# Kernel tuning notes

Measured on AMD Instinct MI355X. Metric: run time of the kernel, lower is better.

## Reference

```python
import jax, jax.numpy as jnp
import numpy as np

B, S, E, H = 16, 512, 768, 12
D = E // H
SCALING = 1.0 / np.sqrt(D * 1.0)  # scaling_factor = 1


def setup_inputs() -> dict:
    key = jax.random.key(0)
    ks = jax.random.split(key, 8)
    query = jax.random.normal(ks[0], (B, S, E), dtype=jnp.float32)
    key_in = jax.random.normal(ks[1], (B, S, E), dtype=jnp.float32)
    value = jax.random.normal(ks[2], (B, S, E), dtype=jnp.float32)
    key_padding_mask = jax.random.randint(ks[3], (B, S), 0, 2).astype(jnp.bool_)
    attn_bias = jax.random.normal(ks[4], (B, H, S, S), dtype=jnp.float32)
    # Learned params. NOTE: original code applies wq to q, k AND v (wk/wv unused).
    Wq = jax.random.normal(ks[5], (E, E), dtype=jnp.float32) * (1.0 / np.sqrt(E))
    bq = jnp.zeros((E,), dtype=jnp.float32)
    Wo = jax.random.normal(ks[6], (E, E), dtype=jnp.float32) * (1.0 / np.sqrt(E))
    bo = jnp.zeros((E,), dtype=jnp.float32)
    return {"query": query, "key": key_in, "value": value,
            "key_padding_mask": key_padding_mask, "attn_bias": attn_bias,
            "Wq": Wq, "bq": bq, "Wo": Wo, "bo": bo}


def _split_heads(x):
    # [B,S,E] -> [B,H,S,D]
    return x.reshape(B, S, H, D).transpose(0, 2, 1, 3)


def reference(query, key, value, key_padding_mask, attn_bias, Wq, bq, Wo, bo):
    q = (query @ Wq + bq) * jnp.asarray(SCALING, query.dtype)
    k = key @ Wq + bq      # faithful: wq used for k and v in the source
    v = value @ Wq + bq
    q, k, v = _split_heads(q), _split_heads(k), _split_heads(v)  # [B,H,S,D]
    w = jnp.einsum('bhtd,bhsd->bhts', q, k)                      # [B,H,T,S]
    w = jnp.where(key_padding_mask[:, None, None, :], -jnp.inf, w)
    w = w + attn_bias
    attn = jax.nn.softmax(w, axis=-1)  # dropout is no-op (training=False)
    o = jnp.einsum('bhts,bhsd->bhtd', attn, v)
    o = o.transpose(0, 2, 1, 3).reshape(B, S, E)
    o = o @ Wo + bo
    attn_weights = w.reshape(B * H, S, S)
    return (o, attn_weights, attn.reshape(B * H, S, S))
```

## Files before the change

### kernel.cpp

```cpp
#include <hip/hip_runtime.h>
#include <cmath>

#define BB 16
#define SS 512
#define EE 768
#define HH 12
#define DD 64
#define NBH (BB*HH)

#define MASK_NEG (-1.0e30f)

__device__ __forceinline__ unsigned short bf16_rn(float x) {
    unsigned u = __float_as_uint(x);
    u += 0x7FFFu + ((u >> 16) & 1u);
    return (unsigned short)(u >> 16);
}
__device__ __forceinline__ float bf16_tof(unsigned short h) {
    return __uint_as_float(((unsigned)h) << 16);
}

typedef __attribute__((ext_vector_type(8))) short bf16x8;
typedef __attribute__((ext_vector_type(4))) float f32x4;
typedef __attribute__((ext_vector_type(4))) unsigned short u16x4;

__global__ __launch_bounds__(256) void conv_w_kernel(
    const float* __restrict__ Wq, const float* __restrict__ Wo,
    unsigned short* __restrict__ wtq, unsigned short* __restrict__ wto)
{
    const float* __restrict__ W = blockIdx.z ? Wo : Wq;
    unsigned short* __restrict__ wt = blockIdx.z ? wto : wtq;
    const int k = blockIdx.x * 256 + threadIdx.x;
    const int n = blockIdx.y;
    const float x = W[(size_t)k * EE + n];
    const unsigned short h = bf16_rn(x);
    const float r = x - bf16_tof(h);
    const unsigned short m = bf16_rn(r);
    const float l2 = r - bf16_tof(m);
    const unsigned short l = bf16_rn(l2);
    const size_t PL = (size_t)EE * EE;
    wt[0 * PL + (size_t)n * EE + k] = h;
    wt[1 * PL + (size_t)n * EE + k] = m;
    wt[2 * PL + (size_t)n * EE + k] = l;
}

__global__ __launch_bounds__(256) void split_gemm_qkv_kernel(
    const float* __restrict__ Xq, const float* __restrict__ Xk,
    const float* __restrict__ Xv, const unsigned short* __restrict__ wt,
    const float* __restrict__ bvec,
    unsigned short* __restrict__ qp, unsigned short* __restrict__ kp,
    unsigned short* __restrict__ vtp)
{
    const int z = blockIdx.z;
    const float* __restrict__ X = (z == 1) ? Xk : (z == 2) ? Xv : Xq;
    const float scale = (z == 0) ? 0.125f : 1.0f;

    const int m0 = blockIdx.x * 128;
    const int n0 = blockIdx.y * 128;

    __shared__ __align__(16) unsigned short lds[4 * 4096];
    const int AH = 0, AL = 4096, BH = 8192, BL = 12288;

    const int tid = threadIdx.x;
    const int srow = tid >> 2;
    const int sg   = tid & 3;
    const int wv = tid >> 6;
    const int wr = wv >> 1, wc = wv & 1;
    const int lane = tid & 63;
    const int l15 = lane & 15, lg = lane >> 4;

    const size_t PL = (size_t)EE * EE;
    const size_t PS = (size_t)NBH * SS * DD;

    f32x4 acc[4][4];
#pragma unroll
    for (int i = 0; i < 4; ++i)
#pragma unroll
        for (int j = 0; j < 4; ++j) acc[i][j] = (f32x4){0.f, 0.f, 0.f, 0.f};

    float4 xf[2][2];
    bf16x8 wh[2], wl[2];

#define QKV_LOAD(K0)                                                          \
    {                                                                         \
        _Pragma("unroll")                                                     \
        for (int half = 0; half < 2; ++half) {                                \
            const int row = srow + 64 * half;                                 \
            const float* xp = &X[(size_t)(m0 + row) * EE + (K0) + sg * 8];    \
            xf[half][0] = *reinterpret_cast<const float4*>(xp);               \
            xf[half][1] = *reinterpret_cast<const float4*>(xp + 4);           \
            const size_t bo = (size_t)(n0 + row) * EE + (K0) + sg * 8;        \
            wh[half] = *reinterpret_cast<const bf16x8*>(&wt[0 * PL + bo]);    \
            wl[half] = *reinterpret_cast<const bf16x8*>(&wt[1 * PL + bo]);    \
        }                                                                     \
    }

    QKV_LOAD(0);

#pragma unroll 1
    for (int k0 = 0; k0 < EE; k0 += 32) {
        __syncthreads();
#pragma unroll
        for (int half = 0; half < 2; ++half) {
            const int row = srow + 64 * half;
            const float xs[8] = {xf[half][0].x, xf[half][0].y, xf[half][0].z, xf[half][0].w,
                                 xf[half][1].x, xf[half][1].y, xf[half][1].z, xf[half][1].w};
            bf16x8 hv, mv;
#pragma unroll
            for (int e = 0; e < 8; ++e) {
                const float x = xs[e];
                const unsigned short h = bf16_rn(x);
                const unsigned short m = bf16_rn(x - bf16_tof(h));
                hv[e] = (short)h;
                mv[e] = (short)m;
            }
            const int o = row * 32 + sg * 8;
            *reinterpret_cast<bf16x8*>(&lds[AH + o]) = hv;
            *reinterpret_cast<bf16x8*>(&lds[AL + o]) = mv;
            *reinterpret_cast<bf16x8*>(&lds[BH + o]) = wh[half];
            *reinterpret_cast<bf16x8*>(&lds[BL + o]) = wl[half];
        }
        __syncthreads();

        if (k0 + 32 < EE) QKV_LOAD(k0 + 32);

        bf16x8 ah[4], al[4];
#pragma unroll
        for (int i = 0; i < 4; ++i) {
            const int o = (wr * 64 + i * 16 + l15) * 32 + lg * 8;
            ah[i] = *reinterpret_cast<const bf16x8*>(&lds[AH + o]);
            al[i] = *reinterpret_cast<const bf16x8*>(&lds[AL + o]);
        }
#pragma unroll
        for (int j = 0; j < 4; ++j) {
            const int o = (wc * 64 + j * 16 + l15) * 32 + lg * 8;
            const bf16x8 bh = *reinterpret_cast<const bf16x8*>(&lds[BH + o]);
            const bf16x8 bl = *reinterpret_cast<const bf16x8*>(&lds[BL + o]);
#pragma unroll
            for (int i = 0; i < 4; ++i) {
                acc[i][j] = __builtin_amdgcn_mfma_f32_16x16x32_bf16(ah[i], bh, acc[i][j], 0, 0, 0);
                acc[i][j] = __builtin_amdgcn_mfma_f32_16x16x32_bf16(ah[i], bl, acc[i][j], 0, 0, 0);
                acc[i][j] = __builtin_amdgcn_mfma_f32_16x16x32_bf16(al[i], bh, acc[i][j], 0, 0, 0);
                acc[i][j] = __builtin_amdgcn_mfma_f32_16x16x32_bf16(al[i], bl, acc[i][j], 0, 0, 0);
            }
        }
    }
#undef QKV_LOAD

    unsigned short* __restrict__ dstp = (z == 0) ? qp : kp;
#pragma unroll
    for (int j = 0; j < 4; ++j) {
        const int n = n0 + wc * 64 + j * 16 + l15;
        const float bvn = bvec[n];
        const int h = n >> 6, d = n & 63;
#pragma unroll
        for (int i = 0; i < 4; ++i) {
            const int mb = m0 + wr * 64 + i * 16 + lg * 4;
#pragma unroll
            for (int r = 0; r < 4; ++r) {
                const int m = mb + r;
                const int bh_ = (m >> 9) * HH + h;
                const int srow_ = m & 511;
                const float val = (acc[i][j][r] + bvn) * scale;
                const unsigned short hi = bf16_rn(val);
                const unsigned short lo = bf16_rn(val - bf16_tof(hi));
                if (z == 2) {
                    const size_t o = ((size_t)bh_ * DD + d) * SS + srow_;
                    vtp[o] = hi;
                    vtp[o + PS] = lo;
                } else {
                    const size_t o = ((size_t)bh_ * SS + srow_) * DD + d;
                    dstp[o] = hi;
                    dstp[o + PS] = lo;
                }
            }
        }
    }
}

__global__ __launch_bounds__(256) void flash_attn_kernel(
    const unsigned short* __restrict__ qp, const unsigned short* __restrict__ kp,
    const unsigned short* __restrict__ vt, const unsigned char* __restrict__ mask,
    const float* __restrict__ bias, float* __restrict__ wout,
    float* __restrict__ ohb, float* __restrict__ stat_m,
    float* __restrict__ stat_inv)
{
    const int bh = blockIdx.y;
    const int b = bh / HH, h = bh % HH;
    const int t0 = blockIdx.x * 64;
    const int tid = threadIdx.x;
    const int wv = tid >> 6;
    const int lane = tid & 63, l15 = lane & 15, lg = lane >> 4;
    const size_t PS = (size_t)NBH * SS * DD;

    __shared__ __align__(16) unsigned short kbuf[2 * 64 * 68];
    __shared__ __align__(16) unsigned short vbuf[2 * 64 * 68];
    __shared__ __align__(16) unsigned short pbuf[4 * 2 * 16 * 68];

    bf16x8 bqh[2], bql[2];
    {
        const unsigned short* qbase = &qp[((size_t)bh * SS + t0 + wv * 16) * DD];
#pragma unroll
        for (int kc = 0; kc < 2; ++kc) {
            const size_t o = (size_t)l15 * DD + kc * 32 + lg * 8;
            bqh[kc] = *reinterpret_cast<const bf16x8*>(&qbase[o]);
            bql[kc] = *reinterpret_cast<const bf16x8*>(&qbase[o + PS]);
        }
    }

    float rm = -3.0e38f, rs = 0.0f;

    f32x4 oac[4];
#pragma unroll
    for (int j = 0; j < 4; ++j) oac[j] = (f32x4){0.f, 0.f, 0.f, 0.f};

    const int t = t0 + wv * 16 + l15;

    const unsigned short* __restrict__ kb0 = &kp[(size_t)bh * SS * DD];
    const unsigned short* __restrict__ vb0 = &vt[(size_t)bh * DD * SS];
    const int srow2 = tid >> 3, sg2 = (tid & 7) * 8;

    bf16x8 krh[2], krl[2], vrh[2], vrl[2];

#define FA_LOADKV(SC)                                                         \
    {                                                                         \
        _Pragma("unroll")                                                     \
        for (int rep = 0; rep < 2; ++rep) {                                   \
            const int row = srow2 + rep * 32;                                 \
            krh[rep] = *reinterpret_cast<const bf16x8*>(                      \
                &kb0[(size_t)((SC) + row) * DD + sg2]);                       \
            krl[rep] = *reinterpret_cast<const bf16x8*>(                      \
                &kb0[(size_t)((SC) + row) * DD + sg2 + PS]);                  \
            vrh[rep] = *reinterpret_cast<const bf16x8*>(                      \
                &vb0[(size_t)row * SS + (SC) + sg2]);                         \
            vrl[rep] = *reinterpret_cast<const bf16x8*>(                      \
                &vb0[(size_t)row * SS + (SC) + sg2 + PS]);                    \
        }                                                                     \
    }

    FA_LOADKV(0);

#pragma unroll 1
    for (int c = 0; c < 8; ++c) {
        const int sc = c * 64;
        __syncthreads();

#pragma unroll
        for (int rep = 0; rep < 2; ++rep) {
            const int row = srow2 + rep * 32;
            *reinterpret_cast<bf16x8*>(&kbuf[row * 68 + sg2]) = krh[rep];
            *reinterpret_cast<bf16x8*>(&kbuf[64 * 68 + row * 68 + sg2]) = krl[rep];
            *reinterpret_cast<bf16x8*>(&vbuf[row * 68 + sg2]) = vrh[rep];
            *reinterpret_cast<bf16x8*>(&vbuf[64 * 68 + row * 68 + sg2]) = vrl[rep];
        }
        __syncthreads();

        if (c < 7) FA_LOADKV(sc + 64);

        float4 bvr[4];
        uchar4 mkr[4];
#pragma unroll
        for (int i = 0; i < 4; ++i) {
            const int s = sc + i * 16 + lg * 4;
            bvr[i] = *reinterpret_cast<const float4*>(&bias[((size_t)bh * SS + t) * SS + s]);
            mkr[i] = *reinterpret_cast<const uchar4*>(&mask[b * SS + s]);
        }

        f32x4 ws[4];
#pragma unroll
        for (int i = 0; i < 4; ++i) ws[i] = (f32x4){0.f, 0.f, 0.f, 0.f};
#pragma unroll
        for (int kc = 0; kc < 2; ++kc) {
#pragma unroll
            for (int i = 0; i < 4; ++i) {
                const int o = (i * 16 + l15) * 68 + kc * 32 + lg * 8;
                const bf16x8 ah = *reinterpret_cast<const bf16x8*>(&kbuf[o]);
                const bf16x8 al = *reinterpret_cast<const bf16x8*>(&kbuf[64 * 68 + o]);
                ws[i] = __builtin_amdgcn_mfma_f32_16x16x32_bf16(ah, bqh[kc], ws[i], 0, 0, 0);
                ws[i] = __builtin_amdgcn_mfma_f32_16x16x32_bf16(ah, bql[kc], ws[i], 0, 0, 0);
                ws[i] = __builtin_amdgcn_mfma_f32_16x16x32_bf16(al, bqh[kc], ws[i], 0, 0, 0);
                ws[i] = __builtin_amdgcn_mfma_f32_16x16x32_bf16(al, bql[kc], ws[i], 0, 0, 0);
            }
        }

        float mx = -3.0e38f;
#pragma unroll
        for (int i = 0; i < 4; ++i) {
            const int s = sc + i * 16 + lg * 4;
            const size_t go = ((size_t)bh * SS + t) * SS + s;
            float4 w4;
            w4.x = mkr[i].x ? MASK_NEG : ws[i][0] + bvr[i].x;
            w4.y = mkr[i].y ? MASK_NEG : ws[i][1] + bvr[i].y;
            w4.z = mkr[i].z ? MASK_NEG : ws[i][2] + bvr[i].z;
            w4.w = mkr[i].w ? MASK_NEG : ws[i][3] + bvr[i].w;
            *reinterpret_cast<float4*>(&wout[go]) = w4;
            ws[i][0] = w4.x; ws[i][1] = w4.y; ws[i][2] = w4.z; ws[i][3] = w4.w;
            mx = fmaxf(mx, fmaxf(fmaxf(w4.x, w4.y), fmaxf(w4.z, w4.w)));
        }
        mx = fmaxf(mx, __shfl_xor(mx, 16));
        mx = fmaxf(mx, __shfl_xor(mx, 32));

        const float m_new = fmaxf(rm, mx);
        float sm = 0.0f;
#pragma unroll
        for (int i = 0; i < 4; ++i)
#pragma unroll
            for (int r = 0; r < 4; ++r) sm += __expf(ws[i][r] - m_new);
        sm += __shfl_xor(sm, 16);
        sm += __shfl_xor(sm, 32);
        const float scl = __expf(rm - m_new);
        rs = rs * scl + sm;
        rm = m_new;

        unsigned short* pw = &pbuf[(wv * 2) * 16 * 68];
#pragma unroll
        for (int i = 0; i < 4; ++i) {
            float4 p4;
            p4.x = __expf(ws[i][0] - m_new);
            p4.y = __expf(ws[i][1] - m_new);
            p4.z = __expf(ws[i][2] - m_new);
            p4.w = __expf(ws[i][3] - m_new);
            u16x4 hv, lv;
            hv.x = bf16_rn(p4.x); lv.x = bf16_rn(p4.x - bf16_tof(hv.x));
            hv.y = bf16_rn(p4.y); lv.y = bf16_rn(p4.y - bf16_tof(hv.y));
            hv.z = bf16_rn(p4.z); lv.z = bf16_rn(p4.z - bf16_tof(hv.z));
            hv.w = bf16_rn(p4.w); lv.w = bf16_rn(p4.w - bf16_tof(hv.w));
            const int po = l15 * 68 + i * 16 + lg * 4;
            *reinterpret_cast<u16x4*>(&pw[po]) = hv;
            *reinterpret_cast<u16x4*>(&pw[16 * 68 + po]) = lv;
        }

        float sclr[4];
#pragma unroll
        for (int r = 0; r < 4; ++r) sclr[r] = __shfl(scl, lg * 4 + r);
#pragma unroll
        for (int j = 0; j < 4; ++j)
#pragma unroll
            for (int r = 0; r < 4; ++r) oac[j][r] *= sclr[r];

#pragma unroll
        for (int kc = 0; kc < 2; ++kc) {
            const int ko = kc * 32 + lg * 8;
            const bf16x8 pah = *reinterpret_cast<const bf16x8*>(&pw[l15 * 68 + ko]);
            const bf16x8 pal = *reinterpret_cast<const bf16x8*>(&pw[16 * 68 + l15 * 68 + ko]);
#pragma unroll
            for (int j = 0; j < 4; ++j) {
                const int o = (j * 16 + l15) * 68 + ko;
                const bf16x8 vh = *reinterpret_cast<const bf16x8*>(&vbuf[o]);
                const bf16x8 vl = *reinterpret_cast<const bf16x8*>(&vbuf[64 * 68 + o]);
                oac[j] = __builtin_amdgcn_mfma_f32_16x16x32_bf16(pah, vh, oac[j], 0, 0, 0);
                oac[j] = __builtin_amdgcn_mfma_f32_16x16x32_bf16(pah, vl, oac[j], 0, 0, 0);
                oac[j] = __builtin_amdgcn_mfma_f32_16x16x32_bf16(pal, vh, oac[j], 0, 0, 0);
                oac[j] = __builtin_amdgcn_mfma_f32_16x16x32_bf16(pal, vl, oac[j], 0, 0, 0);
            }
        }
    }
#undef FA_LOADKV

    const float inv = 1.0f / rs;
    if (lg == 0) {
        stat_m[(size_t)bh * SS + t] = rm;
        stat_inv[(size_t)bh * SS + t] = inv;
    }
    float invr[4];
#pragma unroll
    for (int r = 0; r < 4; ++r) invr[r] = __shfl(inv, lg * 4 + r);
#pragma unroll
    for (int j = 0; j < 4; ++j)
#pragma unroll
        for (int r = 0; r < 4; ++r) {
            const int tr = t0 + wv * 16 + lg * 4 + r;
            ohb[((size_t)b * SS + tr) * EE + h * DD + j * 16 + l15] = oac[j][r] * invr[r];
        }
}

__global__ __launch_bounds__(256) void finish_kernel(
    const float* __restrict__ X, const unsigned short* __restrict__ wt,
    const float* __restrict__ bvec, float* __restrict__ dflat,
    const float* __restrict__ win, const float* __restrict__ stat_m,
    const float* __restrict__ stat_inv, float* __restrict__ attn)
{
    __shared__ __align__(16) unsigned short lds[6 * 4096];

    if (blockIdx.x >= 384) {
        const int nb = gridDim.x - 384;
        const size_t total = (size_t)NBH * SS * (SS / 4);
        for (size_t g = (size_t)(blockIdx.x - 384) * 256 + threadIdx.x; g < total;
             g += (size_t)nb * 256) {
            const size_t row = g >> 7;
            const float m_ = stat_m[row];
            const float iv = stat_inv[row];
            const float4 w4 = reinterpret_cast<const float4*>(win)[g];
            float4 p4;
            p4.x = __expf(w4.x - m_) * iv;
            p4.y = __expf(w4.y - m_) * iv;
            p4.z = __expf(w4.z - m_) * iv;
            p4.w = __expf(w4.w - m_) * iv;
            reinterpret_cast<float4*>(attn)[g] = p4;
        }
        return;
    }

    const int m0 = (blockIdx.x & 63) * 128;
    const int n0 = (blockIdx.x >> 6) * 128;

    const int AH = 0, AM = 4096, AL = 8192, BH = 12288, BM = 16384, BL = 20480;

    const int tid = threadIdx.x;
    const int srow = tid >> 2;
    const int sg   = tid & 3;
    const int wv = tid >> 6;
    const int wr = wv >> 1, wc = wv & 1;
    const int lane = tid & 63;
    const int l15 = lane & 15, lg = lane >> 4;
    const size_t PL = (size_t)EE * EE;

    f32x4 acc[4][4];
#pragma unroll
    for (int i = 0; i < 4; ++i)
#pragma unroll
        for (int j = 0; j < 4; ++j) acc[i][j] = (f32x4){0.f, 0.f, 0.f, 0.f};

#pragma unroll 1
    for (int k0 = 0; k0 < EE; k0 += 32) {
#pragma unroll
        for (int half = 0; half < 2; ++half) {
            const int row = srow + 64 * half;
            const float* xp = &X[(size_t)(m0 + row) * EE + k0 + sg * 8];
            const float4 f0 = *reinterpret_cast<const float4*>(xp);
            const float4 f1 = *reinterpret_cast<const float4*>(xp + 4);
            const float xs[8] = {f0.x, f0.y, f0.z, f0.w, f1.x, f1.y, f1.z, f1.w};
            bf16x8 hv, mv, lv;
#pragma unroll
            for (int e = 0; e < 8; ++e) {
                const float x = xs[e];
                const unsigned short h = bf16_rn(x);
                const float r = x - bf16_tof(h);
                const unsigned short m = bf16_rn(r);
                const float l2 = r - bf16_tof(m);
                hv[e] = (short)h;
                mv[e] = (short)m;
                lv[e] = (short)bf16_rn(l2);
            }
            const int o = row * 32 + sg * 8;
            *reinterpret_cast<bf16x8*>(&lds[AH + o]) = hv;
            *reinterpret_cast<bf16x8*>(&lds[AM + o]) = mv;
            *reinterpret_cast<bf16x8*>(&lds[AL + o]) = lv;

            const size_t bo = (size_t)(n0 + row) * EE + k0 + sg * 8;
            *reinterpret_cast<bf16x8*>(&lds[BH + o]) =
                *reinterpret_cast<const bf16x8*>(&wt[0 * PL + bo]);
            *reinterpret_cast<bf16x8*>(&lds[BM + o]) =
                *reinterpret_cast<const bf16x8*>(&wt[1 * PL + bo]);
            *reinterpret_cast<bf16x8*>(&lds[BL + o]) =
                *reinterpret_cast<const bf16x8*>(&wt[2 * PL + bo]);
        }
        __syncthreads();

        bf16x8 ah[4], am[4], al[4];
#pragma unroll
        for (int i = 0; i < 4; ++i) {
            const int o = (wr * 64 + i * 16 + l15) * 32 + lg * 8;
            ah[i] = *reinterpret_cast<const bf16x8*>(&lds[AH + o]);
            am[i] = *reinterpret_cast<const bf16x8*>(&lds[AM + o]);
            al[i] = *reinterpret_cast<const bf16x8*>(&lds[AL + o]);
        }
#pragma unroll
        for (int j = 0; j < 4; ++j) {
            const int o = (wc * 64 + j * 16 + l15) * 32 + lg * 8;
            const bf16x8 bh = *reinterpret_cast<const bf16x8*>(&lds[BH + o]);
            const bf16x8 bm = *reinterpret_cast<const bf16x8*>(&lds[BM + o]);
            const bf16x8 bl = *reinterpret_cast<const bf16x8*>(&lds[BL + o]);
#pragma unroll
            for (int i = 0; i < 4; ++i) {
                acc[i][j] = __builtin_amdgcn_mfma_f32_16x16x32_bf16(ah[i], bh, acc[i][j], 0, 0, 0);
                acc[i][j] = __builtin_amdgcn_mfma_f32_16x16x32_bf16(ah[i], bm, acc[i][j], 0, 0, 0);
                acc[i][j] = __builtin_amdgcn_mfma_f32_16x16x32_bf16(am[i], bh, acc[i][j], 0, 0, 0);
                acc[i][j] = __builtin_amdgcn_mfma_f32_16x16x32_bf16(ah[i], bl, acc[i][j], 0, 0, 0);
                acc[i][j] = __builtin_amdgcn_mfma_f32_16x16x32_bf16(al[i], bh, acc[i][j], 0, 0, 0);
                acc[i][j] = __builtin_amdgcn_mfma_f32_16x16x32_bf16(am[i], bm, acc[i][j], 0, 0, 0);
            }
        }
        __syncthreads();
    }

#pragma unroll
    for (int j = 0; j < 4; ++j) {
        const int n = n0 + wc * 64 + j * 16 + l15;
        const float bvn = bvec[n];
#pragma unroll
        for (int i = 0; i < 4; ++i) {
            const int mb = m0 + wr * 64 + i * 16 + lg * 4;
#pragma unroll
            for (int r = 0; r < 4; ++r)
                dflat[(size_t)(mb + r) * EE + n] = acc[i][j][r] + bvn;
        }
    }
}

__global__ __launch_bounds__(256) void proj_kernel(
    const float* __restrict__ Xq, const float* __restrict__ Xk,
    const float* __restrict__ Xv, const float* __restrict__ W,
    const float* __restrict__ bvec, float* __restrict__ qb,
    float* __restrict__ kb, float* __restrict__ vb)
{
    const int z = blockIdx.z;
    const float* __restrict__ X = (z == 0) ? Xq : (z == 1) ? Xk : Xv;
    float* __restrict__ Dst = (z == 0) ? qb : (z == 1) ? kb : vb;
    const float scale = (z == 0) ? 0.125f : 1.0f;

    const int m0 = blockIdx.x * 128;
    const int n0 = blockIdx.y * 128;

    __shared__ float As[16][128];
    __shared__ float Bs[16][128];

    const int tid = threadIdx.x;
    const int ty = tid >> 4, tx = tid & 15;

    float acc[8][8];
#pragma unroll
    for (int i = 0; i < 8; ++i)
#pragma unroll
        for (int j = 0; j < 8; ++j) acc[i][j] = 0.0f;

    const int arow = tid >> 1;
    const int ak   = (tid & 1) * 8;
    const int brow = tid >> 4;
    const int bn   = (tid & 15) * 8;

    for (int k0 = 0; k0 < EE; k0 += 16) {
        const float4* ap = reinterpret_cast<const float4*>(&X[(size_t)(m0 + arow) * EE + k0 + ak]);
        float4 a0 = ap[0], a1 = ap[1];
        As[ak + 0][arow] = a0.x; As[ak + 1][arow] = a0.y;
        As[ak + 2][arow] = a0.z; As[ak + 3][arow] = a0.w;
        As[ak + 4][arow] = a1.x; As[ak + 5][arow] = a1.y;
        As[ak + 6][arow] = a1.z; As[ak + 7][arow] = a1.w;

        const float4* bp = reinterpret_cast<const float4*>(&W[(size_t)(k0 + brow) * EE + n0 + bn]);
        float4 b0 = bp[0], b1 = bp[1];
        *reinterpret_cast<float4*>(&Bs[brow][bn])     = b0;
        *reinterpret_cast<float4*>(&Bs[brow][bn + 4]) = b1;
        __syncthreads();

#pragma unroll
        for (int kk = 0; kk < 16; ++kk) {
            float4 aA = *reinterpret_cast<const float4*>(&As[kk][ty * 8]);
            float4 aB = *reinterpret_cast<const float4*>(&As[kk][ty * 8 + 4]);
            float4 bA = *reinterpret_cast<const float4*>(&Bs[kk][tx * 8]);
            float4 bB = *reinterpret_cast<const float4*>(&Bs[kk][tx * 8 + 4]);
            float av[8] = {aA.x, aA.y, aA.z, aA.w, aB.x, aB.y, aB.z, aB.w};
            float bv[8] = {bA.x, bA.y, bA.z, bA.w, bB.x, bB.y, bB.z, bB.w};
#pragma unroll
            for (int i = 0; i < 8; ++i)
#pragma unroll
                for (int j = 0; j < 8; ++j)
                    acc[i][j] = fmaf(av[i], bv[j], acc[i][j]);
        }
        __syncthreads();
    }

    const int nbase = n0 + tx * 8;
    float bq8[8];
    {
        float4 c0 = *reinterpret_cast<const float4*>(&bvec[nbase]);
        float4 c1 = *reinterpret_cast<const float4*>(&bvec[nbase + 4]);
        bq8[0]=c0.x; bq8[1]=c0.y; bq8[2]=c0.z; bq8[3]=c0.w;
        bq8[4]=c1.x; bq8[5]=c1.y; bq8[6]=c1.z; bq8[7]=c1.w;
    }
    const int hh = nbase >> 6;
    const int dd = nbase & 63;
#pragma unroll
    for (int i = 0; i < 8; ++i) {
        const int m = m0 + ty * 8 + i;
        const int bidx = m >> 9;
        const int srow = m & 511;
        float* dst = &Dst[(((size_t)bidx * HH + hh) * SS + srow) * DD + dd];
        float4 v0, v1;
        v0.x = (acc[i][0] + bq8[0]) * scale;
        v0.y = (acc[i][1] + bq8[1]) * scale;
        v0.z = (acc[i][2] + bq8[2]) * scale;
        v0.w = (acc[i][3] + bq8[3]) * scale;
        v1.x = (acc[i][4] + bq8[4]) * scale;
        v1.y = (acc[i][5] + bq8[5]) * scale;
        v1.z = (acc[i][6] + bq8[6]) * scale;
        v1.w = (acc[i][7] + bq8[7]) * scale;
        *reinterpret_cast<float4*>(dst)     = v0;
        *reinterpret_cast<float4*>(dst + 4) = v1;
    }
}

__global__ __launch_bounds__(256) void scores_kernel(
    const float* __restrict__ qb, const float* __restrict__ kb,
    const unsigned char* __restrict__ mask,
    const float* __restrict__ bias, float* __restrict__ wout)
{
    const int bh = blockIdx.z;
    const int b  = bh / HH;
    const int t0 = blockIdx.y * 128;
    const int s0 = blockIdx.x * 128;

    __shared__ float As[16][128];
    __shared__ float Bs[16][128];

    const int tid = threadIdx.x;
    const int ty = tid >> 4, tx = tid & 15;

    float acc[8][8];
#pragma unroll
    for (int i = 0; i < 8; ++i)
#pragma unroll
        for (int j = 0; j < 8; ++j) acc[i][j] = 0.0f;

    const int arow = tid >> 1;
    const int ak   = (tid & 1) * 8;

    const float* __restrict__ qbase = &qb[(size_t)bh * SS * DD];
    const float* __restrict__ kbase = &kb[(size_t)bh * SS * DD];

    for (int k0 = 0; k0 < DD; k0 += 16) {
        const float4* ap = reinterpret_cast<const float4*>(&qbase[(size_t)(t0 + arow) * DD + k0 + ak]);
        float4 a0 = ap[0], a1 = ap[1];
        As[ak + 0][arow] = a0.x; As[ak + 1][arow] = a0.y;
        As[ak + 2][arow] = a0.z; As[ak + 3][arow] = a0.w;
        As[ak + 4][arow] = a1.x; As[ak + 5][arow] = a1.y;
        As[ak + 6][arow] = a1.z; As[ak + 7][arow] = a1.w;

        const float4* bp = reinterpret_cast<const float4*>(&kbase[(size_t)(s0 + arow) * DD + k0 + ak]);
        float4 b0 = bp[0], b1 = bp[1];
        Bs[ak + 0][arow] = b0.x; Bs[ak + 1][arow] = b0.y;
        Bs[ak + 2][arow] = b0.z; Bs[ak + 3][arow] = b0.w;
        Bs[ak + 4][arow] = b1.x; Bs[ak + 5][arow] = b1.y;
        Bs[ak + 6][arow] = b1.z; Bs[ak + 7][arow] = b1.w;
        __syncthreads();

#pragma unroll
        for (int kk = 0; kk < 16; ++kk) {
            float4 aA = *reinterpret_cast<const float4*>(&As[kk][ty * 8]);
            float4 aB = *reinterpret_cast<const float4*>(&As[kk][ty * 8 + 4]);
            float4 bA = *reinterpret_cast<const float4*>(&Bs[kk][tx * 8]);
            float4 bB = *reinterpret_cast<const float4*>(&Bs[kk][tx * 8 + 4]);
            float av[8] = {aA.x, aA.y, aA.z, aA.w, aB.x, aB.y, aB.z, aB.w};
            float bv[8] = {bA.x, bA.y, bA.z, bA.w, bB.x, bB.y, bB.z, bB.w};
#pragma unroll
            for (int i = 0; i < 8; ++i)
#pragma unroll
                for (int j = 0; j < 8; ++j)
                    acc[i][j] = fmaf(av[i], bv[j], acc[i][j]);
        }
        __syncthreads();
    }

    const int scol = s0 + tx * 8;
    const uint2 mv = *reinterpret_cast<const uint2*>(&mask[b * SS + scol]);
    bool msk[8];
    msk[0] = (mv.x & 0x000000ffu) != 0;
    msk[1] = (mv.x & 0x0000ff00u) != 0;
    msk[2] = (mv.x & 0x00ff0000u) != 0;
    msk[3] = (mv.x & 0xff000000u) != 0;
    msk[4] = (mv.y & 0x000000ffu) != 0;
    msk[5] = (mv.y & 0x0000ff00u) != 0;
    msk[6] = (mv.y & 0x00ff0000u) != 0;
    msk[7] = (mv.y & 0xff000000u) != 0;
#pragma unroll
    for (int i = 0; i < 8; ++i) {
        const int t = t0 + ty * 8 + i;
        const float4 bv0 = *reinterpret_cast<const float4*>(&bias[((size_t)bh * SS + t) * SS + scol]);
        const float4 bv1 = *reinterpret_cast<const float4*>(&bias[((size_t)bh * SS + t) * SS + scol + 4]);
        float4 w0, w1;
        w0.x = msk[0] ? MASK_NEG : acc[i][0] + bv0.x;
        w0.y = msk[1] ? MASK_NEG : acc[i][1] + bv0.y;
        w0.z = msk[2] ? MASK_NEG : acc[i][2] + bv0.z;
        w0.w = msk[3] ? MASK_NEG : acc[i][3] + bv0.w;
        w1.x = msk[4] ? MASK_NEG : acc[i][4] + bv1.x;
        w1.y = msk[5] ? MASK_NEG : acc[i][5] + bv1.y;
        w1.z = msk[6] ? MASK_NEG : acc[i][6] + bv1.z;
        w1.w = msk[7] ? MASK_NEG : acc[i][7] + bv1.w;
        float* wrow = &wout[((size_t)bh * SS + t) * SS + scol];
        *reinterpret_cast<float4*>(wrow)     = w0;
        *reinterpret_cast<float4*>(wrow + 4) = w1;
    }
}

__global__ __launch_bounds__(256) void softmax_pv_kernel(
    const float* __restrict__ win, const float* __restrict__ vb,
    float* __restrict__ attn, float* __restrict__ ohb)
{
    const int bh = blockIdx.y;
    const int b = bh / HH, h = bh % HH;
    const int t0 = blockIdx.x * 64;
    const int wave = threadIdx.x >> 6;
    const int lane = threadIdx.x & 63;

    __shared__ float pws[4][8][512];

#pragma unroll 1
    for (int g = 0; g < 2; ++g) {
        const int tb = t0 + wave * 16 + g * 8;

#pragma unroll 1
        for (int r = 0; r < 8; ++r) {
            const int t = tb + r;
            const float4* wp = reinterpret_cast<const float4*>(&win[((size_t)bh * SS + t) * SS + lane * 8]);
            float4 w0 = wp[0], w1 = wp[1];
            float wv[8] = {w0.x,w0.y,w0.z,w0.w,w1.x,w1.y,w1.z,w1.w};
            float mx = wv[0];
#pragma unroll
            for (int j = 1; j < 8; ++j) mx = fmaxf(mx, wv[j]);
#pragma unroll
            for (int off = 32; off > 0; off >>= 1)
                mx = fmaxf(mx, __shfl_xor(mx, off));
            float e[8];
            float sum = 0.0f;
#pragma unroll
            for (int j = 0; j < 8; ++j) { e[j] = __expf(wv[j] - mx); sum += e[j]; }
#pragma unroll
            for (int off = 32; off > 0; off >>= 1)
                sum += __shfl_xor(sum, off);
            const float inv = 1.0f / sum;
            float4 p0, p1;
            p0.x = e[0]*inv; p0.y = e[1]*inv; p0.z = e[2]*inv; p0.w = e[3]*inv;
            p1.x = e[4]*inv; p1.y = e[5]*inv; p1.z = e[6]*inv; p1.w = e[7]*inv;
            float* arow = &attn[((size_t)bh * SS + t) * SS + lane * 8];
            *reinterpret_cast<float4*>(arow)     = p0;
            *reinterpret_cast<float4*>(arow + 4) = p1;
            *reinterpret_cast<float4*>(&pws[wave][r][lane * 8])     = p0;
            *reinterpret_cast<float4*>(&pws[wave][r][lane * 8 + 4]) = p1;
        }
        __syncthreads();

        float oacc[8] = {0,0,0,0,0,0,0,0};
#pragma unroll 2
        for (int s = 0; s < SS; s += 4) {
            const float v0 = vb[((size_t)bh * SS + s + 0) * DD + lane];
            const float v1 = vb[((size_t)bh * SS + s + 1) * DD + lane];
            const float v2 = vb[((size_t)bh * SS + s + 2) * DD + lane];
            const float v3 = vb[((size_t)bh * SS + s + 3) * DD + lane];
#pragma unroll
            for (int r = 0; r < 8; ++r) {
                const float4 p4 = *reinterpret_cast<const float4*>(&pws[wave][r][s]);
                oacc[r] = fmaf(p4.x, v0, oacc[r]);
                oacc[r] = fmaf(p4.y, v1, oacc[r]);
                oacc[r] = fmaf(p4.z, v2, oacc[r]);
                oacc[r] = fmaf(p4.w, v3, oacc[r]);
            }
        }
#pragma unroll
        for (int r = 0; r < 8; ++r)
            ohb[((size_t)b * SS + tb + r) * EE + h * DD + lane] = oacc[r];
        __syncthreads();
    }
}

__global__ __launch_bounds__(256) void outproj_kernel(
    const float* __restrict__ A, const float* __restrict__ W,
    const float* __restrict__ bvec, float* __restrict__ out)
{
    const int m0 = blockIdx.x * 128;
    const int n0 = blockIdx.y * 128;

    __shared__ float As[16][128];
    __shared__ float Bs[16][128];

    const int tid = threadIdx.x;
    const int ty = tid >> 4, tx = tid & 15;

    float acc[8][8];
#pragma unroll
    for (int i = 0; i < 8; ++i)
#pragma unroll
        for (int j = 0; j < 8; ++j) acc[i][j] = 0.0f;

    const int arow = tid >> 1;
    const int ak   = (tid & 1) * 8;
    const int brow = tid >> 4;
    const int bn   = (tid & 15) * 8;

    for (int k0 = 0; k0 < EE; k0 += 16) {
        const float4* ap = reinterpret_cast<const float4*>(&A[(size_t)(m0 + arow) * EE + k0 + ak]);
        float4 a0 = ap[0], a1 = ap[1];
        As[ak + 0][arow] = a0.x; As[ak + 1][arow] = a0.y;
        As[ak + 2][arow] = a0.z; As[ak + 3][arow] = a0.w;
        As[ak + 4][arow] = a1.x; As[ak + 5][arow] = a1.y;
        As[ak + 6][arow] = a1.z; As[ak + 7][arow] = a1.w;

        const float4* bp = reinterpret_cast<const float4*>(&W[(size_t)(k0 + brow) * EE + n0 + bn]);
        float4 b0 = bp[0], b1 = bp[1];
        *reinterpret_cast<float4*>(&Bs[brow][bn])     = b0;
        *reinterpret_cast<float4*>(&Bs[brow][bn + 4]) = b1;
        __syncthreads();

#pragma unroll
        for (int kk = 0; kk < 16; ++kk) {
            float4 aA = *reinterpret_cast<const float4*>(&As[kk][ty * 8]);
            float4 aB = *reinterpret_cast<const float4*>(&As[kk][ty * 8 + 4]);
            float4 bA = *reinterpret_cast<const float4*>(&Bs[kk][tx * 8]);
            float4 bB = *reinterpret_cast<const float4*>(&Bs[kk][tx * 8 + 4]);
            float av[8] = {aA.x, aA.y, aA.z, aA.w, aB.x, aB.y, aB.z, aB.w};
            float bv[8] = {bA.x, bA.y, bA.z, bA.w, bB.x, bB.y, bB.z, bB.w};
#pragma unroll
            for (int i = 0; i < 8; ++i)
#pragma unroll
                for (int j = 0; j < 8; ++j)
                    acc[i][j] = fmaf(av[i], bv[j], acc[i][j]);
        }
        __syncthreads();
    }

    const int nbase = n0 + tx * 8;
    float bq8[8];
    {
        float4 c0 = *reinterpret_cast<const float4*>(&bvec[nbase]);
        float4 c1 = *reinterpret_cast<const float4*>(&bvec[nbase + 4]);
        bq8[0]=c0.x; bq8[1]=c0.y; bq8[2]=c0.z; bq8[3]=c0.w;
        bq8[4]=c1.x; bq8[5]=c1.y; bq8[6]=c1.z; bq8[7]=c1.w;
    }
#pragma unroll
    for (int i = 0; i < 8; ++i) {
        const int m = m0 + ty * 8 + i;
        float* dst = &out[(size_t)m * EE + nbase];
        float4 v0, v1;
        v0.x = acc[i][0] + bq8[0]; v0.y = acc[i][1] + bq8[1];
        v0.z = acc[i][2] + bq8[2]; v0.w = acc[i][3] + bq8[3];
        v1.x = acc[i][4] + bq8[4]; v1.y = acc[i][5] + bq8[5];
        v1.z = acc[i][6] + bq8[6]; v1.w = acc[i][7] + bq8[7];
        *reinterpret_cast<float4*>(dst)     = v0;
        *reinterpret_cast<float4*>(dst + 4) = v1;
    }
}

extern "C" void kernel_launch(void* const* d_in, const int* in_sizes, int n_in,
                              void* d_out, int out_size, void* d_ws, size_t ws_size,
                              hipStream_t stream)
{
    const float* query = (const float*)d_in[0];
    const float* key   = (const float*)d_in[1];
    const float* value = (const float*)d_in[2];
    const unsigned char* mask = (const unsigned char*)d_in[3];
    const float* bias  = (const float*)d_in[4];
    const float* Wq    = (const float*)d_in[5];
    const float* bq    = (const float*)d_in[6];
    const float* Wo    = (const float*)d_in[7];
    const float* bo    = (const float*)d_in[8];

    float* out_o = (float*)d_out;
    float* out_w = out_o + (size_t)BB * SS * EE;
    float* out_a = out_w + (size_t)NBH * SS * SS;

    const size_t headsz = (size_t)NBH * SS * DD;
    const size_t wt_elems = 3 * (size_t)EE * EE;

    const size_t need_mfma = 3 * (2 * headsz * sizeof(unsigned short))
                           + headsz * sizeof(float)
                           + 2 * wt_elems * sizeof(unsigned short);

    if (ws_size >= need_mfma) {
        unsigned short* qp = (unsigned short*)d_ws;
        unsigned short* kp = qp + 2 * headsz;
        unsigned short* vt = kp + 2 * headsz;
        float* ohb = (float*)(vt + 2 * headsz);
        unsigned short* wtq = (unsigned short*)(ohb + headsz);
        unsigned short* wto = wtq + wt_elems;
        float* stat_m   = (float*)wtq;
        float* stat_inv = stat_m + (size_t)NBH * SS;

        conv_w_kernel<<<dim3(3, EE, 2), 256, 0, stream>>>(Wq, Wo, wtq, wto);
        split_gemm_qkv_kernel<<<dim3(64, 6, 3), 256, 0, stream>>>(
            query, key, value, wtq, bq, qp, kp, vt);
        flash_attn_kernel<<<dim3(8, NBH), 256, 0, stream>>>(
            qp, kp, vt, mask, bias, out_w, ohb, stat_m, stat_inv);
        finish_kernel<<<384 + 2048, 256, 0, stream>>>(
            ohb, wto, bo, out_o, out_w, stat_m, stat_inv, out_a);
    } else {
        const size_t base_bytes = 4 * headsz * sizeof(float);
        if (ws_size < base_bytes) return;
        float* qb  = (float*)d_ws;
        float* kb  = qb + headsz;
        float* vb  = kb + headsz;
        float* ohb = vb + headsz;
        proj_kernel<<<dim3(64, 6, 3), 256, 0, stream>>>(query, key, value, Wq, bq, qb, kb, vb);
        scores_kernel<<<dim3(4, 4, NBH), 256, 0, stream>>>(qb, kb, mask, bias, out_w);
        softmax_pv_kernel<<<dim3(8, NBH), 256, 0, stream>>>(out_w, vb, out_a, ohb);
        outproj_kernel<<<dim3(64, 6), 256, 0, stream>>>(ohb, Wo, bo, out_o);
    }
}
```

Baseline: 439.1 us.

## Build P operand via lane shuffles instead of LDS staging, raise occupancy hint

Removes the per-wave shared-memory buffer for the probability tile and builds the MFMA A operand directly from registers using cross-lane shuffles. The exponentials are computed once and reused for both the row sum and P, where they were previously computed twice. The bias load is moved next to its use, and the launch bounds ask for 4 blocks per CU. This frees LDS and may raise occupancy, but it adds many shuffle instructions and could cause register spilling under the tighter register budget.

New measurement: 475.0 us. +8.2%, slower.

```diff
diff --git a/kernel.cpp b/kernel.cpp
--- a/kernel.cpp
+++ b/kernel.cpp
@@ -177,7 +177,7 @@
     }
 }
 
-__global__ __launch_bounds__(256) void flash_attn_kernel(
+__global__ __launch_bounds__(256, 4) void flash_attn_kernel(
     const unsigned short* __restrict__ qp, const unsigned short* __restrict__ kp,
     const unsigned short* __restrict__ vt, const unsigned char* __restrict__ mask,
     const float* __restrict__ bias, float* __restrict__ wout,
@@ -194,7 +194,6 @@
 
     __shared__ __align__(16) unsigned short kbuf[2 * 64 * 68];
     __shared__ __align__(16) unsigned short vbuf[2 * 64 * 68];
-    __shared__ __align__(16) unsigned short pbuf[4 * 2 * 16 * 68];
 
     bf16x8 bqh[2], bql[2];
     {
@@ -256,14 +255,10 @@
 
         if (c < 7) FA_LOADKV(sc + 64);
 
-        float4 bvr[4];
         uchar4 mkr[4];
 #pragma unroll
-        for (int i = 0; i < 4; ++i) {
-            const int s = sc + i * 16 + lg * 4;
-            bvr[i] = *reinterpret_cast<const float4*>(&bias[((size_t)bh * SS + t) * SS + s]);
-            mkr[i] = *reinterpret_cast<const uchar4*>(&mask[b * SS + s]);
-        }
+        for (int i = 0; i < 4; ++i)
+            mkr[i] = *reinterpret_cast<const uchar4*>(&mask[b * SS + sc + i * 16 + lg * 4]);
 
         f32x4 ws[4];
 #pragma unroll
@@ -287,11 +282,12 @@
         for (int i = 0; i < 4; ++i) {
             const int s = sc + i * 16 + lg * 4;
             const size_t go = ((size_t)bh * SS + t) * SS + s;
+            const float4 bv = *reinterpret_cast<const float4*>(&bias[go]);
             float4 w4;
-            w4.x = mkr[i].x ? MASK_NEG : ws[i][0] + bvr[i].x;
-            w4.y = mkr[i].y ? MASK_NEG : ws[i][1] + bvr[i].y;
-            w4.z = mkr[i].z ? MASK_NEG : ws[i][2] + bvr[i].z;
-            w4.w = mkr[i].w ? MASK_NEG : ws[i][3] + bvr[i].w;
+            w4.x = mkr[i].x ? MASK_NEG : ws[i][0] + bv.x;
+            w4.y = mkr[i].y ? MASK_NEG : ws[i][1] + bv.y;
+            w4.z = mkr[i].z ? MASK_NEG : ws[i][2] + bv.z;
+            w4.w = mkr[i].w ? MASK_NEG : ws[i][3] + bv.w;
             *reinterpret_cast<float4*>(&wout[go]) = w4;
             ws[i][0] = w4.x; ws[i][1] = w4.y; ws[i][2] = w4.z; ws[i][3] = w4.w;
             mx = fmaxf(mx, fmaxf(fmaxf(w4.x, w4.y), fmaxf(w4.z, w4.w)));
@@ -300,35 +296,23 @@
         mx = fmaxf(mx, __shfl_xor(mx, 32));
 
         const float m_new = fmaxf(rm, mx);
+#pragma unroll
+        for (int i = 0; i < 4; ++i) {
+            ws[i][0] = __expf(ws[i][0] - m_new);
+            ws[i][1] = __expf(ws[i][1] - m_new);
+            ws[i][2] = __expf(ws[i][2] - m_new);
+            ws[i][3] = __expf(ws[i][3] - m_new);
+        }
         float sm = 0.0f;
 #pragma unroll
         for (int i = 0; i < 4; ++i)
-#pragma unroll
-            for (int r = 0; r < 4; ++r) sm += __expf(ws[i][r] - m_new);
+            sm += (ws[i][0] + ws[i][1]) + (ws[i][2] + ws[i][3]);
         sm += __shfl_xor(sm, 16);
         sm += __shfl_xor(sm, 32);
         const float scl = __expf(rm - m_new);
         rs = rs * scl + sm;
         rm = m_new;
 
-        unsigned short* pw = &pbuf[(wv * 2) * 16 * 68];
-#pragma unroll
-        for (int i = 0; i < 4; ++i) {
-            float4 p4;
-            p4.x = __expf(ws[i][0] - m_new);
-            p4.y = __expf(ws[i][1] - m_new);
-            p4.z = __expf(ws[i][2] - m_new);
-            p4.w = __expf(ws[i][3] - m_new);
-            u16x4 hv, lv;
-            hv.x = bf16_rn(p4.x); lv.x = bf16_rn(p4.x - bf16_tof(hv.x));
-            hv.y = bf16_rn(p4.y); lv.y = bf16_rn(p4.y - bf16_tof(hv.y));
-            hv.z = bf16_rn(p4.z); lv.z = bf16_rn(p4.z - bf16_tof(hv.z));
-            hv.w = bf16_rn(p4.w); lv.w = bf16_rn(p4.w - bf16_tof(hv.w));
-            const int po = l15 * 68 + i * 16 + lg * 4;
-            *reinterpret_cast<u16x4*>(&pw[po]) = hv;
-            *reinterpret_cast<u16x4*>(&pw[16 * 68 + po]) = lv;
-        }
-
         float sclr[4];
 #pragma unroll
         for (int r = 0; r < 4; ++r) sclr[r] = __shfl(scl, lg * 4 + r);
@@ -337,11 +321,27 @@
 #pragma unroll
             for (int r = 0; r < 4; ++r) oac[j][r] *= sclr[r];
 
+        const int srcA = l15 + 16 * ((2 * lg) & 3);
+        const int srcB = l15 + 16 * ((2 * lg + 1) & 3);
 #pragma unroll
         for (int kc = 0; kc < 2; ++kc) {
+            bf16x8 pah, pal;
+#pragma unroll
+            for (int r = 0; r < 4; ++r) {
+                const float vA0 = __shfl(ws[2 * kc + 0][r], srcA);
+                const float vA1 = __shfl(ws[2 * kc + 1][r], srcA);
+                const float vB0 = __shfl(ws[2 * kc + 0][r], srcB);
+                const float vB1 = __shfl(ws[2 * kc + 1][r], srcB);
+                const float ga = (lg < 2) ? vA0 : vA1;
+                const float gb = (lg < 2) ? vB0 : vB1;
+                const unsigned short ha = bf16_rn(ga);
+                const unsigned short hb = bf16_rn(gb);
+                pah[r]     = (short)ha;
+                pah[4 + r] = (short)hb;
+                pal[r]     = (short)bf16_rn(ga - bf16_tof(ha));
+                pal[4 + r] = (short)bf16_rn(gb - bf16_tof(hb));
+            }
             const int ko = kc * 32 + lg * 8;
-            const bf16x8 pah = *reinterpret_cast<const bf16x8*>(&pw[l15 * 68 + ko]);
-            const bf16x8 pal = *reinterpret_cast<const bf16x8*>(&pw[16 * 68 + l15 * 68 + ko]);
 #pragma unroll
             for (int j = 0; j < 4; ++j) {
                 const int o = (j * 16 + l15) * 68 + ko;
```
